# Kernel optimization log

Measured on AMD Instinct MI355X. Metric: run time of the kernel, lower is better.

The kernel has to match this reference:

```python
import jax, jax.numpy as jnp
import numpy as np
from jax import lax

B, N, D = 4, 2048, 1024
MAX_SEQ = 2048
GROUPS = 4  # math.gcd(1024, 4)
LN_EPS = 1e-5


def setup_inputs() -> dict:
    key = jax.random.key(0)
    ks = jax.random.split(key, 12)
    s = 0.02
    return {
        "x": jax.random.normal(ks[0], (B, N, D), jnp.float32),
        "Wq": jax.random.normal(ks[1], (D, D), jnp.float32) * s,
        "Wk": jax.random.normal(ks[2], (D, D), jnp.float32) * s,
        "Wv": jax.random.normal(ks[3], (D, D), jnp.float32) * s,
        "rel_bias": jax.random.normal(ks[4], (1, MAX_SEQ, MAX_SEQ), jnp.float32) * s,
        "conv_w": jax.random.normal(ks[5], (D, D // GROUPS, 3), jnp.float32) * s,
        "conv_b": jnp.zeros((D,), jnp.float32),
        "resg_w": jax.random.normal(ks[6], (D, D), jnp.float32) * s,
        "resg_b": jnp.zeros((D,), jnp.float32),
        "ln_g": jnp.ones((D,), jnp.float32),
        "ln_b": jnp.zeros((D,), jnp.float32),
        "fc1_w": jax.random.normal(ks[7], (D // 2, D), jnp.float32) * s,
        "fc1_b": jnp.zeros((D // 2,), jnp.float32),
        "fc2_w": jax.random.normal(ks[8], (1, D // 2), jnp.float32) * s,
        "fc2_b": jnp.zeros((1,), jnp.float32),
    }


def _forward(x, Wq, Wk, Wv, rel_bias, conv_w, conv_b, resg_w, resg_b,
             ln_g, ln_b, fc1_w, fc1_b, fc2_w, fc2_b):
    b, n, d = x.shape
    scale = 1.0 / jnp.sqrt(jnp.asarray(d, x.dtype))
    q = x @ Wq.T  # [b,n,dk]
    k = x @ Wk.T
    v = x @ Wv.T  # [b,n,dv]
    att = jnp.einsum("bqd,bkd->bqk", q, k) * scale + rel_bias[:, :n, :n]
    causal = jnp.tril(jnp.ones((n, n), bool))
    att = jnp.where(causal, att, jnp.asarray(-jnp.inf, att.dtype))
    att = jax.nn.softmax(att, axis=-1)  # dropout is identity at eval
    att_out = jnp.einsum("bqk,bkd->bqd", att, v)
    # grouped temporal conv over sequence dim: v [b,n,dv] -> NCH [b,dv,n]
    conv = lax.conv_general_dilated(
        v.transpose(0, 2, 1), conv_w, window_strides=(1,), padding=[(1, 1)],
        dimension_numbers=("NCH", "OIH", "NCH"), feature_group_count=GROUPS)
    conv = conv + conv_b[None, :, None]
    out = att_out + conv.transpose(0, 2, 1)
    res = jax.nn.sigmoid(out @ resg_w.T + resg_b)
    out = x + res * out
    mu = out.mean(-1, keepdims=True)
    var = out.var(-1, keepdims=True)
    out = (out - mu) * lax.rsqrt(var + LN_EPS) * ln_g + ln_b
    h = jax.nn.gelu(out @ fc1_w.T + fc1_b, approximate=False)
    return jax.nn.sigmoid(h @ fc2_w.T + fc2_b)


def reference(x, Wq, Wk, Wv, rel_bias, conv_w, conv_b, resg_w, resg_b,
              ln_g, ln_b, fc1_w, fc1_b, fc2_w, fc2_b):
    return _forward(x, Wq, Wk, Wv, rel_bias, conv_w, conv_b, resg_w, resg_b,
                    ln_g, ln_b, fc1_w, fc1_b, fc2_w, fc2_b)
```

## Files before the change

### kernel.cpp

```cpp
#include <hip/hip_runtime.h>
#include <math.h>

#define NSEQ 2048
#define DDIM 1024
#define BSZ  4
#define BM 128
#define BN 128
#define BK 64

typedef short bf16x8 __attribute__((ext_vector_type(8)));
typedef float f32x4 __attribute__((ext_vector_type(4)));
typedef unsigned int u32;
typedef unsigned short u16;

__device__ __forceinline__ u16 f2bf(float f) {
  union { float f; u32 u; } x; x.f = f;
  u32 r = x.u + 0x7FFFu + ((x.u >> 16) & 1u);
  return (u16)(r >> 16);
}
__device__ __forceinline__ float bf2f(u16 h) {
  union { u32 u; float f; } x; x.u = ((u32)h) << 16; return x.f;
}
__device__ __forceinline__ float sigmoidf_(float x) {
  return 1.0f / (1.0f + expf(-x));
}

__device__ __forceinline__ void async_copy16(const u16* g, u16* l) {
  __builtin_amdgcn_global_load_lds(
      (const __attribute__((address_space(1))) u32*)g,
      (__attribute__((address_space(3))) u32*)l, 16, 0, 0);
}

__device__ __forceinline__ void stage_tile(const u16* __restrict__ gsrc, size_t ld,
                                           int k0, u16* lds, int tid) {
  const int wave = tid >> 6, lane = tid & 63;
  const int rr = lane >> 3;
  const int q  = (lane & 7) ^ rr;
#pragma unroll
  for (int j = 0; j < 4; ++j) {
    const int c = j * 4 + wave;
    async_copy16(gsrc + (size_t)(c * 8 + rr) * ld + k0 + q * 8, lds + c * 512);
  }
}

__device__ __forceinline__ void mfma_step(const u16* Al, const u16* Bl,
                                          int wr, int wc, int l16, int quad,
                                          f32x4 acc[4][4]) {
  const int r7 = l16 & 7;
#pragma unroll
  for (int ks = 0; ks < 2; ++ks) {
    const int s = ((ks * 4 + quad) ^ r7) << 3;
    bf16x8 a[4], b[4];
#pragma unroll
    for (int i = 0; i < 4; ++i) {
      a[i] = *(const bf16x8*)(Al + (wr * 64 + i * 16 + l16) * BK + s);
      b[i] = *(const bf16x8*)(Bl + (wc * 64 + i * 16 + l16) * BK + s);
    }
#pragma unroll
    for (int i = 0; i < 4; ++i)
#pragma unroll
      for (int j = 0; j < 4; ++j)
        acc[i][j] = __builtin_amdgcn_mfma_f32_16x16x32_bf16(a[i], b[j], acc[i][j], 0, 0, 0);
  }
}

__device__ __forceinline__ void zero_acc(f32x4 acc[4][4]) {
#pragma unroll
  for (int i = 0; i < 4; ++i)
#pragma unroll
    for (int j = 0; j < 4; ++j) {
      f32x4 z = {0.f, 0.f, 0.f, 0.f};
      acc[i][j] = z;
    }
}

__device__ __forceinline__ void gemm_loop(const u16* A, size_t lda,
                                          const u16* Bt, size_t ldb, int K,
                                          u16* Al, u16* Bl, int tid,
                                          int wr, int wc, int l16, int quad,
                                          f32x4 acc[4][4]) {
  for (int k0 = 0; k0 < K; k0 += BK) {
    __syncthreads();
    stage_tile(A, lda, k0, Al, tid);
    stage_tile(Bt, ldb, k0, Bl, tid);
    __syncthreads();
    mfma_step(Al, Bl, wr, wc, l16, quad, acc);
  }
}

#define ATT_PB 2228224

__global__ __launch_bounds__(256) void k_prep(
    const float* __restrict__ x,  const float* __restrict__ Wq,
    const float* __restrict__ Wk, const float* __restrict__ Wv,
    const float* __restrict__ rw, const float* __restrict__ f1w,
    const float* __restrict__ cw,
    u16* __restrict__ xb,  u16* __restrict__ Wqb, u16* __restrict__ Wkb,
    u16* __restrict__ Wvb, u16* __restrict__ rwb, u16* __restrict__ f1wb,
    u16* __restrict__ cwp, u16* __restrict__ vpad, float* __restrict__ outz)
{
  const int blk = blockIdx.x, tid = threadIdx.x;
  const float* s; u16* d; int base;
  if (blk < 8192)       { s = x;   d = xb;   base = blk; }
  else if (blk < 9216)  { s = Wq;  d = Wqb;  base = blk - 8192; }
  else if (blk < 10240) { s = Wk;  d = Wkb;  base = blk - 9216; }
  else if (blk < 11264) { s = Wv;  d = Wvb;  base = blk - 10240; }
  else if (blk < 12288) { s = rw;  d = rwb;  base = blk - 11264; }
  else if (blk < 12800) { s = f1w; d = f1wb; base = blk - 12288; }
  else if (blk < 13824) {
    const int o = blk - 12800, i = tid;
#pragma unroll
    for (int tap = 0; tap < 3; ++tap)
      cwp[(size_t)o * 768 + tap * 256 + i] = f2bf(cw[(size_t)o * 768 + i * 3 + tap]);
    return;
  } else if (blk < 13832) {
    const int e = blk - 13824, bb = e >> 1, which = e & 1;
    u16* row = vpad + (size_t)bb * 2050 * 1024 + (which ? (size_t)2049 * 1024 : 0);
    ushort4 z = {0, 0, 0, 0};
    ((ushort4*)row)[tid] = z;
    return;
  } else {
    const int e = blk - 13832;
    float4 z = {0.f, 0.f, 0.f, 0.f};
    ((float4*)outz)[e * 256 + tid] = z;
    return;
  }
  const int i = base * 256 + tid;
  const float4 v = ((const float4*)s)[i];
  ushort4 o;
  o.x = f2bf(v.x); o.y = f2bf(v.y); o.z = f2bf(v.z); o.w = f2bf(v.w);
  ((ushort4*)d)[i] = o;
}

__global__ __launch_bounds__(256) void k_qkv(
    const u16* __restrict__ xb, const u16* __restrict__ Wqb,
    const u16* __restrict__ Wkb, const u16* __restrict__ Wvb,
    u16* __restrict__ qb, u16* __restrict__ kb, u16* __restrict__ vpad)
{
  __shared__ u16 Al[BM * BK], Bl[BN * BK];
  const int tid = threadIdx.x, z = blockIdx.z;
  const u16* W = (z == 0) ? Wqb : ((z == 1) ? Wkb : Wvb);
  const int row0 = blockIdx.x * BM, col0 = blockIdx.y * BN;
  const int lane = tid & 63, wave = tid >> 6;
  const int quad = lane >> 4, l16 = lane & 15, wr = wave >> 1, wc = wave & 1;
  f32x4 acc[4][4];
  zero_acc(acc);
  gemm_loop(xb + (size_t)row0 * DDIM, DDIM, W + (size_t)col0 * DDIM, DDIM, DDIM,
            Al, Bl, tid, wr, wc, l16, quad, acc);
#pragma unroll
  for (int mi = 0; mi < 4; ++mi)
#pragma unroll
    for (int r = 0; r < 4; ++r) {
      const int grow = row0 + wr * 64 + mi * 16 + quad * 4 + r;
#pragma unroll
      for (int ni = 0; ni < 4; ++ni) {
        const int gcol = col0 + wc * 64 + ni * 16 + l16;
        const u16 hv = f2bf(acc[mi][ni][r]);
        if (z == 2) {
          const int b = grow >> 11, t = grow & 2047;
          vpad[(size_t)b * 2050 * 1024 + 1024 + (size_t)t * 1024 + gcol] = hv;
        } else {
          (z == 0 ? qb : kb)[(size_t)grow * DDIM + gcol] = hv;
        }
      }
    }
}

__global__ __launch_bounds__(256) void k_vt(const u16* __restrict__ vpad,
                                            u16* __restrict__ vT)
{
  __shared__ u16 tile[64][72];
  const int t0 = blockIdx.x * 64, d0 = blockIdx.y * 64, b = blockIdx.z;
  const int tid = threadIdx.x;
  const u16* vb = vpad + (size_t)b * 2050 * 1024 + 1024;
#pragma unroll
  for (int p = 0; p < 4; ++p) {
    const int r = p * 16 + (tid >> 4), c = (tid & 15) << 2;
    const ushort4 v4 = *(const ushort4*)(vb + (size_t)(t0 + r) * 1024 + d0 + c);
    tile[r][c] = v4.x; tile[r][c + 1] = v4.y; tile[r][c + 2] = v4.z; tile[r][c + 3] = v4.w;
  }
  __syncthreads();
  u16* ob = vT + (size_t)b * DDIM * NSEQ;
#pragma unroll
  for (int p = 0; p < 4; ++p) {
    const int d = p * 16 + (tid >> 4), t = (tid & 15) << 2;
    ushort4 o;
    o.x = tile[t][d]; o.y = tile[t + 1][d]; o.z = tile[t + 2][d]; o.w = tile[t + 3][d];
    *(ushort4*)(ob + (size_t)(d0 + d) * NSEQ + t0 + t) = o;
  }
}

__global__ __launch_bounds__(256) void k_conv(
    const u16* __restrict__ vpad, const u16* __restrict__ cwp,
    const float* __restrict__ cb, u16* __restrict__ convb)
{
  __shared__ u16 Al[BM * BK], Bl[BN * BK];
  const int tid = threadIdx.x;
  const int row0 = blockIdx.x * BM;
  const int col0 = blockIdx.y * BN;
  const int g = col0 >> 8;
  const int b = row0 >> 11, t0 = row0 & 2047;
  const u16* vb = vpad + (size_t)b * 2050 * 1024 + 1024;
  const u16* Bbase = cwp + (size_t)col0 * 768;
  const int lane = tid & 63, wave = tid >> 6;
  const int quad = lane >> 4, l16 = lane & 15, wr = wave >> 1, wc = wave & 1;
  const int rr = lane >> 3;
  const int q  = (lane & 7) ^ rr;
  const int gch = g << 8;
  f32x4 acc[4][4];
  zero_acc(acc);
  for (int k0 = 0; k0 < 768; k0 += BK) {
    __syncthreads();
    const int tap = k0 >> 8;
    const int i0 = k0 & 255;
#pragma unroll
    for (int j = 0; j < 4; ++j) {
      const int c = j * 4 + wave;
      const int r = c * 8 + rr;
      async_copy16(vb + (size_t)(t0 + r - 1 + tap) * 1024 + gch + i0 + q * 8,
                   Al + c * 512);
    }
    stage_tile(Bbase, 768, k0, Bl, tid);
    __syncthreads();
    mfma_step(Al, Bl, wr, wc, l16, quad, acc);
  }
#pragma unroll
  for (int mi = 0; mi < 4; ++mi)
#pragma unroll
    for (int r = 0; r < 4; ++r) {
      const int grow = row0 + wr * 64 + mi * 16 + quad * 4 + r;
#pragma unroll
      for (int ni = 0; ni < 4; ++ni) {
        const int gcol = col0 + wc * 64 + ni * 16 + l16;
        convb[(size_t)grow * DDIM + gcol] = f2bf(cb[gcol] + acc[mi][ni][r]);
      }
    }
}

__global__ __launch_bounds__(256) void k_scores(
    const u16* __restrict__ qb, const u16* __restrict__ kb,
    const float* __restrict__ rb, float* __restrict__ attp)
{
  __shared__ u16 Al[BM * BK], Bl[BN * BK];
  const int b = blockIdx.x, t = blockIdx.y, tid = threadIdx.x;
  int it = 0;
  while ((it + 1) * (it + 2) / 2 <= t) ++it;
  const int jt = t - it * (it + 1) / 2;
  const int row0 = it * BM, col0 = jt * BN;
  const int lane = tid & 63, wave = tid >> 6;
  const int quad = lane >> 4, l16 = lane & 15, wr = wave >> 1, wc = wave & 1;
  f32x4 acc[4][4];
  zero_acc(acc);
  gemm_loop(qb + ((size_t)b * NSEQ + row0) * DDIM, DDIM,
            kb + ((size_t)b * NSEQ + col0) * DDIM, DDIM, DDIM,
            Al, Bl, tid, wr, wc, l16, quad, acc);
  float* abase = attp + (size_t)b * ATT_PB + (size_t)(it * (it + 1) / 2) * 16384;
  const int ldp = (it + 1) * 128;
#pragma unroll
  for (int mi = 0; mi < 4; ++mi)
#pragma unroll
    for (int r = 0; r < 4; ++r) {
      const int ri = wr * 64 + mi * 16 + quad * 4 + r;
      const int gi = row0 + ri;
#pragma unroll
      for (int ni = 0; ni < 4; ++ni) {
        const int j = col0 + wc * 64 + ni * 16 + l16;
        abase[(size_t)ri * ldp + j] =
            acc[mi][ni][r] * 0.03125f + rb[(size_t)gi * NSEQ + j];
      }
    }
}

__global__ __launch_bounds__(256) void k_softmax(const float* __restrict__ attp,
                                                 u16* __restrict__ pp)
{
  const int i = blockIdx.x, b = blockIdx.y;
  const int it = i >> 7;
  const int wlen = (it + 1) << 7;
  const size_t rbase = (size_t)b * ATT_PB +
                       (size_t)(it * (it + 1) / 2) * 16384 + (size_t)(i & 127) * wlen;
  const float* row = attp + rbase;
  u16* orow = pp + rbase;
  const int valid = i + 1;
  const int tid = threadIdx.x;
  const int lane = tid & 63, wid = tid >> 6;

  float v[8];
  float m = -1e30f;
#pragma unroll
  for (int t = 0; t < 8; ++t) {
    const int idx = tid + (t << 8);
    v[t] = (idx < valid) ? row[idx] : -1e30f;
    m = fmaxf(m, v[t]);
  }
#pragma unroll
  for (int off = 32; off; off >>= 1) m = fmaxf(m, __shfl_xor(m, off));
  __shared__ float red[4];
  if (lane == 0) red[wid] = m;
  __syncthreads();
  m = fmaxf(fmaxf(red[0], red[1]), fmaxf(red[2], red[3]));
  __syncthreads();

  float s = 0.f;
#pragma unroll
  for (int t = 0; t < 8; ++t) {
    const int idx = tid + (t << 8);
    float e = (idx < valid) ? expf(v[t] - m) : 0.f;
    v[t] = e;
    s += e;
  }
#pragma unroll
  for (int off = 32; off; off >>= 1) s += __shfl_xor(s, off);
  if (lane == 0) red[wid] = s;
  __syncthreads();
  s = red[0] + red[1] + red[2] + red[3];
  const float inv = 1.0f / s;
#pragma unroll
  for (int t = 0; t < 8; ++t) {
    const int idx = tid + (t << 8);
    if (idx < wlen) orow[idx] = f2bf(v[t] * inv);
  }
}

__global__ __launch_bounds__(256) void k_pv(
    const u16* __restrict__ pp, const u16* __restrict__ vT,
    const u16* __restrict__ convb, u16* __restrict__ buf1b)
{
  __shared__ u16 Al[BM * BK], Bl[BN * BK];
  const int it = 15 - blockIdx.x, nt = blockIdx.y, b = blockIdx.z;
  const int tid = threadIdx.x;
  const int row0 = it * BM, col0 = nt * BN;
  const int K = (it + 1) * BM;
  const int lane = tid & 63, wave = tid >> 6;
  const int quad = lane >> 4, l16 = lane & 15, wr = wave >> 1, wc = wave & 1;
  f32x4 acc[4][4];
  zero_acc(acc);
  gemm_loop(pp + (size_t)b * ATT_PB + (size_t)(it * (it + 1) / 2) * 16384, K,
            vT + ((size_t)b * DDIM + col0) * NSEQ, NSEQ, K,
            Al, Bl, tid, wr, wc, l16, quad, acc);
  const size_t obase = (size_t)b * NSEQ * DDIM;
#pragma unroll
  for (int mi = 0; mi < 4; ++mi)
#pragma unroll
    for (int r = 0; r < 4; ++r) {
      const int grow = row0 + wr * 64 + mi * 16 + quad * 4 + r;
#pragma unroll
      for (int ni = 0; ni < 4; ++ni) {
        const int gcol = col0 + wc * 64 + ni * 16 + l16;
        const size_t idx = obase + (size_t)grow * DDIM + gcol;
        buf1b[idx] = f2bf(acc[mi][ni][r] + bf2f(convb[idx]));
      }
    }
}

__global__ __launch_bounds__(256) void k_resgate(
    const u16* __restrict__ buf1b, const u16* __restrict__ rwb,
    const float* __restrict__ rbias, const u16* __restrict__ xb,
    u16* __restrict__ buf2)
{
  __shared__ u16 Al[BM * BK], Bl[BN * BK];
  const int tid = threadIdx.x;
  const int row0 = blockIdx.x * BM, col0 = blockIdx.y * BN;
  const int lane = tid & 63, wave = tid >> 6;
  const int quad = lane >> 4, l16 = lane & 15, wr = wave >> 1, wc = wave & 1;
  f32x4 acc[4][4];
  zero_acc(acc);
  gemm_loop(buf1b + (size_t)row0 * DDIM, DDIM, rwb + (size_t)col0 * DDIM, DDIM,
            DDIM, Al, Bl, tid, wr, wc, l16, quad, acc);
#pragma unroll
  for (int mi = 0; mi < 4; ++mi)
#pragma unroll
    for (int r = 0; r < 4; ++r) {
      const int grow = row0 + wr * 64 + mi * 16 + quad * 4 + r;
#pragma unroll
      for (int ni = 0; ni < 4; ++ni) {
        const int gcol = col0 + wc * 64 + ni * 16 + l16;
        const size_t idx = (size_t)grow * DDIM + gcol;
        const float gate = sigmoidf_(acc[mi][ni][r] + rbias[gcol]);
        buf2[idx] = f2bf(bf2f(xb[idx]) + gate * bf2f(buf1b[idx]));
      }
    }
}

__global__ __launch_bounds__(256) void k_ln(
    const u16* __restrict__ buf, const float* __restrict__ gw,
    const float* __restrict__ gb, u16* __restrict__ outb)
{
  const int row = blockIdx.x;
  const u16* p = buf + (size_t)row * DDIM;
  const int tid = threadIdx.x;
  const int lane = tid & 63, wid = tid >> 6;
  const int c = tid << 2;
  const ushort4 raw = *(const ushort4*)(p + c);
  float4 val;
  val.x = bf2f(raw.x); val.y = bf2f(raw.y); val.z = bf2f(raw.z); val.w = bf2f(raw.w);
  float s = val.x + val.y + val.z + val.w;
  float s2 = val.x * val.x + val.y * val.y + val.z * val.z + val.w * val.w;
#pragma unroll
  for (int off = 32; off; off >>= 1) {
    s += __shfl_xor(s, off);
    s2 += __shfl_xor(s2, off);
  }
  __shared__ float r1[4], r2[4];
  if (lane == 0) { r1[wid] = s; r2[wid] = s2; }
  __syncthreads();
  s = r1[0] + r1[1] + r1[2] + r1[3];
  s2 = r2[0] + r2[1] + r2[2] + r2[3];
  const float mean = s * (1.0f / DDIM);
  const float var = s2 * (1.0f / DDIM) - mean * mean;
  const float rstd = rsqrtf(var + 1e-5f);
  const float4 g4 = *(const float4*)(gw + c);
  const float4 b4 = *(const float4*)(gb + c);
  ushort4 o;
  o.x = f2bf((val.x - mean) * rstd * g4.x + b4.x);
  o.y = f2bf((val.y - mean) * rstd * g4.y + b4.y);
  o.z = f2bf((val.z - mean) * rstd * g4.z + b4.z);
  o.w = f2bf((val.w - mean) * rstd * g4.w + b4.w);
  *(ushort4*)(outb + (size_t)row * DDIM + c) = o;
}

__global__ __launch_bounds__(256) void k_fc1(
    const u16* __restrict__ A, const u16* __restrict__ W,
    const float* __restrict__ bias, const float* __restrict__ w2,
    float* __restrict__ outacc)
{
  __shared__ u16 Al[BM * BK], Bl[BN * BK];
  const int tid = threadIdx.x;
  const int row0 = blockIdx.x * BM, col0 = blockIdx.y * BN;
  const int lane = tid & 63, wave = tid >> 6;
  const int quad = lane >> 4, l16 = lane & 15, wr = wave >> 1, wc = wave & 1;
  f32x4 acc[4][4];
  zero_acc(acc);
  gemm_loop(A + (size_t)row0 * DDIM, DDIM, W + (size_t)col0 * DDIM, DDIM, DDIM,
            Al, Bl, tid, wr, wc, l16, quad, acc);
  float w4[4], b4[4];
#pragma unroll
  for (int ni = 0; ni < 4; ++ni) {
    const int gcol = col0 + wc * 64 + ni * 16 + l16;
    w4[ni] = w2[gcol];
    b4[ni] = bias[gcol];
  }
#pragma unroll
  for (int mi = 0; mi < 4; ++mi)
#pragma unroll
    for (int r = 0; r < 4; ++r) {
      const int grow = row0 + wr * 64 + mi * 16 + quad * 4 + r;
      float part = 0.f;
#pragma unroll
      for (int ni = 0; ni < 4; ++ni) {
        const float t = acc[mi][ni][r] + b4[ni];
        const float g = 0.5f * t * (1.0f + erff(t * 0.70710678118654752f));
        part = fmaf(g, w4[ni], part);
      }
#pragma unroll
      for (int off = 1; off < 16; off <<= 1) part += __shfl_xor(part, off, 16);
      if (l16 == 0) atomicAdd(outacc + grow, part);
    }
}

__global__ __launch_bounds__(256) void k_fin(float* __restrict__ out,
                                             const float* __restrict__ b2)
{
  const int i = blockIdx.x * 256 + threadIdx.x;
  out[i] = sigmoidf_(out[i] + b2[0]);
}

extern "C" void kernel_launch(void* const* d_in, const int* in_sizes, int n_in,
                              void* d_out, int out_size, void* d_ws, size_t ws_size,
                              hipStream_t stream) {
  const float* x    = (const float*)d_in[0];
  const float* Wq   = (const float*)d_in[1];
  const float* Wk   = (const float*)d_in[2];
  const float* Wv   = (const float*)d_in[3];
  const float* rb   = (const float*)d_in[4];
  const float* cw   = (const float*)d_in[5];
  const float* cb   = (const float*)d_in[6];
  const float* rw   = (const float*)d_in[7];
  const float* rbias= (const float*)d_in[8];
  const float* lng  = (const float*)d_in[9];
  const float* lnb  = (const float*)d_in[10];
  const float* f1w  = (const float*)d_in[11];
  const float* f1b  = (const float*)d_in[12];
  const float* f2w  = (const float*)d_in[13];
  const float* f2b  = (const float*)d_in[14];
  float* out = (float*)d_out;
  char* w8 = (char*)d_ws;

  u16* xb    = (u16*)(w8 + 0);
  u16* Wqb   = (u16*)(w8 + 16777216);
  u16* Wkb   = (u16*)(w8 + 18874368);
  u16* Wvb   = (u16*)(w8 + 20971520);
  u16* rwb   = (u16*)(w8 + 23068672);
  u16* f1wb  = (u16*)(w8 + 25165824);
  u16* cwp   = (u16*)(w8 + 26214400);
  u16* qb    = (u16*)(w8 + 27787264);
  u16* kb    = (u16*)(w8 + 44564480);
  u16* vpad  = (u16*)(w8 + 61341696);
  u16* vT    = (u16*)(w8 + 78135296);
  float* attp= (float*)(w8 + 94912512);
  u16* convb = (u16*)(w8 + 130564096);
  u16* pp    = (u16*)(w8 + 27787264);
  u16* buf1b = (u16*)(w8 + 45613056);
  u16* buf2  = (u16*)(w8 + 94912512);
  u16* ln16  = (u16*)(w8 + 78135296);

  k_prep   <<<dim3(13840),     256, 0, stream>>>(x, Wq, Wk, Wv, rw, f1w, cw,
                                                 xb, Wqb, Wkb, Wvb, rwb, f1wb,
                                                 cwp, vpad, out);
  k_qkv    <<<dim3(64, 8, 3),  256, 0, stream>>>(xb, Wqb, Wkb, Wvb, qb, kb, vpad);
  k_vt     <<<dim3(32, 16, 4), 256, 0, stream>>>(vpad, vT);
  k_conv   <<<dim3(64, 8),     256, 0, stream>>>(vpad, cwp, cb, convb);
  k_scores <<<dim3(4, 136),    256, 0, stream>>>(qb, kb, rb, attp);
  k_softmax<<<dim3(NSEQ, BSZ), 256, 0, stream>>>(attp, pp);
  k_pv     <<<dim3(16, 8, 4),  256, 0, stream>>>(pp, vT, convb, buf1b);
  k_resgate<<<dim3(64, 8),     256, 0, stream>>>(buf1b, rwb, rbias, xb, buf2);
  k_ln     <<<dim3(BSZ * NSEQ),256, 0, stream>>>(buf2, lng, lnb, ln16);
  k_fc1    <<<dim3(64, 4),     256, 0, stream>>>(ln16, f1wb, f1b, f2w, out);
  k_fin    <<<dim3(32),        256, 0, stream>>>(out, f2b);
}
```

Measured before the change: 384.2 us.

## Fold LayerNorm into resgate stats and fc1 epilogue; store scores in fp16

The standalone LayerNorm kernel is removed. Row sum and sum-of-squares are accumulated with atomics in the resgate epilogue. The LN gain is folded into fc1 weights, with per-column sums of W·g and W·b precomputed, so fc1 applies mean and rstd algebraically in its epilogue on the raw residual output. Attention scores are written as fp16 instead of fp32, halving the score buffer traffic between the scores and softmax kernels. The costs are extra atomics, precision risk from computing variance as E[x²]-μ² and from fp16 scores, and an extra pass to zero the stats buffers.

New measurement: 383.1 us. About the same (-0.3%).

```diff
diff --git a/kernel.cpp b/kernel.cpp
--- a/kernel.cpp
+++ b/kernel.cpp
@@ -20,6 +20,12 @@
 }
 __device__ __forceinline__ float bf2f(u16 h) {
   union { u32 u; float f; } x; x.u = ((u32)h) << 16; return x.f;
+}
+__device__ __forceinline__ u16 f2h(float f) {
+  union { _Float16 h; u16 u; } x; x.h = (_Float16)f; return x.u;
+}
+__device__ __forceinline__ float h2f(u16 u) {
+  union { _Float16 h; u16 u; } x; x.u = u; return (float)x.h;
 }
 __device__ __forceinline__ float sigmoidf_(float x) {
   return 1.0f / (1.0f + expf(-x));
@@ -94,39 +100,69 @@
     const float* __restrict__ x,  const float* __restrict__ Wq,
     const float* __restrict__ Wk, const float* __restrict__ Wv,
     const float* __restrict__ rw, const float* __restrict__ f1w,
-    const float* __restrict__ cw,
+    const float* __restrict__ cw, const float* __restrict__ lng,
+    const float* __restrict__ lnb, const float* __restrict__ f1b,
     u16* __restrict__ xb,  u16* __restrict__ Wqb, u16* __restrict__ Wkb,
     u16* __restrict__ Wvb, u16* __restrict__ rwb, u16* __restrict__ f1wb,
-    u16* __restrict__ cwp, u16* __restrict__ vpad, float* __restrict__ outz)
+    u16* __restrict__ cwp, u16* __restrict__ vpad, float* __restrict__ outz,
+    float* __restrict__ lsum, float* __restrict__ s1, float* __restrict__ tb1)
 {
   const int blk = blockIdx.x, tid = threadIdx.x;
-  const float* s; u16* d; int base;
+  if (blk >= 12800) {
+    if (blk < 13824) {
+      const int o = blk - 12800, i = tid;
+#pragma unroll
+      for (int tap = 0; tap < 3; ++tap)
+        cwp[(size_t)o * 768 + tap * 256 + i] = f2bf(cw[(size_t)o * 768 + i * 3 + tap]);
+    } else if (blk < 13832) {
+      const int e = blk - 13824, bb = e >> 1, which = e & 1;
+      u16* row = vpad + (size_t)bb * 2050 * 1024 + (which ? (size_t)2049 * 1024 : 0);
+      ushort4 z = {0, 0, 0, 0};
+      ((ushort4*)row)[tid] = z;
+    } else if (blk < 13840) {
+      const int e = blk - 13832;
+      float4 z = {0.f, 0.f, 0.f, 0.f};
+      ((float4*)outz)[e * 256 + tid] = z;
+    } else if (blk < 13856) {
+      const int e = blk - 13840;
+      float4 z = {0.f, 0.f, 0.f, 0.f};
+      ((float4*)lsum)[e * 256 + tid] = z;
+    } else {
+      const int c = blk - 13856;
+      const float4 w = ((const float4*)f1w)[c * 256 + tid];
+      const float4 g = ((const float4*)lng)[tid];
+      const float4 bb = ((const float4*)lnb)[tid];
+      float s = w.x * g.x + w.y * g.y + w.z * g.z + w.w * g.w;
+      float t = w.x * bb.x + w.y * bb.y + w.z * bb.z + w.w * bb.w;
+      const int lane = tid & 63, wid = tid >> 6;
+#pragma unroll
+      for (int off = 32; off; off >>= 1) {
+        s += __shfl_xor(s, off);
+        t += __shfl_xor(t, off);
+      }
+      __shared__ float r1[4], r2[4];
+      if (lane == 0) { r1[wid] = s; r2[wid] = t; }
+      __syncthreads();
+      if (tid == 0) {
+        s1[c]  = r1[0] + r1[1] + r1[2] + r1[3];
+        tb1[c] = r2[0] + r2[1] + r2[2] + r2[3] + f1b[c];
+      }
+    }
+    return;
+  }
+  const float* s; u16* d; int base; bool scale_g = false;
   if (blk < 8192)       { s = x;   d = xb;   base = blk; }
   else if (blk < 9216)  { s = Wq;  d = Wqb;  base = blk - 8192; }
   else if (blk < 10240) { s = Wk;  d = Wkb;  base = blk - 9216; }
   else if (blk < 11264) { s = Wv;  d = Wvb;  base = blk - 10240; }
   else if (blk < 12288) { s = rw;  d = rwb;  base = blk - 11264; }
-  else if (blk < 12800) { s = f1w; d = f1wb; base = blk - 12288; }
-  else if (blk < 13824) {
-    const int o = blk - 12800, i = tid;
-#pragma unroll
-    for (int tap = 0; tap < 3; ++tap)
-      cwp[(size_t)o * 768 + tap * 256 + i] = f2bf(cw[(size_t)o * 768 + i * 3 + tap]);
-    return;
-  } else if (blk < 13832) {
-    const int e = blk - 13824, bb = e >> 1, which = e & 1;
-    u16* row = vpad + (size_t)bb * 2050 * 1024 + (which ? (size_t)2049 * 1024 : 0);
-    ushort4 z = {0, 0, 0, 0};
-    ((ushort4*)row)[tid] = z;
-    return;
-  } else {
-    const int e = blk - 13832;
-    float4 z = {0.f, 0.f, 0.f, 0.f};
-    ((float4*)outz)[e * 256 + tid] = z;
-    return;
-  }
+  else                  { s = f1w; d = f1wb; base = blk - 12288; scale_g = true; }
   const int i = base * 256 + tid;
-  const float4 v = ((const float4*)s)[i];
+  float4 v = ((const float4*)s)[i];
+  if (scale_g) {
+    const float4 g = ((const float4*)lng)[i & 255];
+    v.x *= g.x; v.y *= g.y; v.z *= g.z; v.w *= g.w;
+  }
   ushort4 o;
   o.x = f2bf(v.x); o.y = f2bf(v.y); o.z = f2bf(v.z); o.w = f2bf(v.w);
   ((ushort4*)d)[i] = o;
@@ -239,7 +275,7 @@
 
 __global__ __launch_bounds__(256) void k_scores(
     const u16* __restrict__ qb, const u16* __restrict__ kb,
-    const float* __restrict__ rb, float* __restrict__ attp)
+    const float* __restrict__ rb, u16* __restrict__ attp)
 {
   __shared__ u16 Al[BM * BK], Bl[BN * BK];
   const int b = blockIdx.x, t = blockIdx.y, tid = threadIdx.x;
@@ -254,7 +290,7 @@
   gemm_loop(qb + ((size_t)b * NSEQ + row0) * DDIM, DDIM,
             kb + ((size_t)b * NSEQ + col0) * DDIM, DDIM, DDIM,
             Al, Bl, tid, wr, wc, l16, quad, acc);
-  float* abase = attp + (size_t)b * ATT_PB + (size_t)(it * (it + 1) / 2) * 16384;
+  u16* abase = attp + (size_t)b * ATT_PB + (size_t)(it * (it + 1) / 2) * 16384;
   const int ldp = (it + 1) * 128;
 #pragma unroll
   for (int mi = 0; mi < 4; ++mi)
@@ -266,12 +302,12 @@
       for (int ni = 0; ni < 4; ++ni) {
         const int j = col0 + wc * 64 + ni * 16 + l16;
         abase[(size_t)ri * ldp + j] =
-            acc[mi][ni][r] * 0.03125f + rb[(size_t)gi * NSEQ + j];
-      }
-    }
-}
-
-__global__ __launch_bounds__(256) void k_softmax(const float* __restrict__ attp,
+            f2h(acc[mi][ni][r] * 0.03125f + rb[(size_t)gi * NSEQ + j]);
+      }
+    }
+}
+
+__global__ __launch_bounds__(256) void k_softmax(const u16* __restrict__ attp,
                                                  u16* __restrict__ pp)
 {
   const int i = blockIdx.x, b = blockIdx.y;
@@ -279,7 +315,7 @@
   const int wlen = (it + 1) << 7;
   const size_t rbase = (size_t)b * ATT_PB +
                        (size_t)(it * (it + 1) / 2) * 16384 + (size_t)(i & 127) * wlen;
-  const float* row = attp + rbase;
+  const u16* row = attp + rbase;
   u16* orow = pp + rbase;
   const int valid = i + 1;
   const int tid = threadIdx.x;
@@ -290,7 +326,7 @@
 #pragma unroll
   for (int t = 0; t < 8; ++t) {
     const int idx = tid + (t << 8);
-    v[t] = (idx < valid) ? row[idx] : -1e30f;
+    v[t] = (idx < valid) ? h2f(row[idx]) : -1e30f;
     m = fmaxf(m, v[t]);
   }
 #pragma unroll
@@ -356,7 +392,7 @@
 __global__ __launch_bounds__(256) void k_resgate(
     const u16* __restrict__ buf1b, const u16* __restrict__ rwb,
     const float* __restrict__ rbias, const u16* __restrict__ xb,
-    u16* __restrict__ buf2)
+    u16* __restrict__ buf2, float* __restrict__ lsum, float* __restrict__ lsum2)
 {
   __shared__ u16 Al[BM * BK], Bl[BN * BK];
   const int tid = threadIdx.x;
@@ -372,57 +408,35 @@
 #pragma unroll
     for (int r = 0; r < 4; ++r) {
       const int grow = row0 + wr * 64 + mi * 16 + quad * 4 + r;
+      float rs = 0.f, rs2 = 0.f;
 #pragma unroll
       for (int ni = 0; ni < 4; ++ni) {
         const int gcol = col0 + wc * 64 + ni * 16 + l16;
         const size_t idx = (size_t)grow * DDIM + gcol;
         const float gate = sigmoidf_(acc[mi][ni][r] + rbias[gcol]);
-        buf2[idx] = f2bf(bf2f(xb[idx]) + gate * bf2f(buf1b[idx]));
-      }
-    }
-}
-
-__global__ __launch_bounds__(256) void k_ln(
-    const u16* __restrict__ buf, const float* __restrict__ gw,
-    const float* __restrict__ gb, u16* __restrict__ outb)
-{
-  const int row = blockIdx.x;
-  const u16* p = buf + (size_t)row * DDIM;
-  const int tid = threadIdx.x;
-  const int lane = tid & 63, wid = tid >> 6;
-  const int c = tid << 2;
-  const ushort4 raw = *(const ushort4*)(p + c);
-  float4 val;
-  val.x = bf2f(raw.x); val.y = bf2f(raw.y); val.z = bf2f(raw.z); val.w = bf2f(raw.w);
-  float s = val.x + val.y + val.z + val.w;
-  float s2 = val.x * val.x + val.y * val.y + val.z * val.z + val.w * val.w;
-#pragma unroll
-  for (int off = 32; off; off >>= 1) {
-    s += __shfl_xor(s, off);
-    s2 += __shfl_xor(s2, off);
-  }
-  __shared__ float r1[4], r2[4];
-  if (lane == 0) { r1[wid] = s; r2[wid] = s2; }
-  __syncthreads();
-  s = r1[0] + r1[1] + r1[2] + r1[3];
-  s2 = r2[0] + r2[1] + r2[2] + r2[3];
-  const float mean = s * (1.0f / DDIM);
-  const float var = s2 * (1.0f / DDIM) - mean * mean;
-  const float rstd = rsqrtf(var + 1e-5f);
-  const float4 g4 = *(const float4*)(gw + c);
-  const float4 b4 = *(const float4*)(gb + c);
-  ushort4 o;
-  o.x = f2bf((val.x - mean) * rstd * g4.x + b4.x);
-  o.y = f2bf((val.y - mean) * rstd * g4.y + b4.y);
-  o.z = f2bf((val.z - mean) * rstd * g4.z + b4.z);
-  o.w = f2bf((val.w - mean) * rstd * g4.w + b4.w);
-  *(ushort4*)(outb + (size_t)row * DDIM + c) = o;
+        const u16 vb = f2bf(bf2f(xb[idx]) + gate * bf2f(buf1b[idx]));
+        buf2[idx] = vb;
+        const float vr = bf2f(vb);
+        rs += vr;
+        rs2 += vr * vr;
+      }
+#pragma unroll
+      for (int off = 1; off < 16; off <<= 1) {
+        rs  += __shfl_xor(rs, off, 16);
+        rs2 += __shfl_xor(rs2, off, 16);
+      }
+      if (l16 == 0) {
+        atomicAdd(lsum + grow, rs);
+        atomicAdd(lsum2 + grow, rs2);
+      }
+    }
 }
 
 __global__ __launch_bounds__(256) void k_fc1(
     const u16* __restrict__ A, const u16* __restrict__ W,
-    const float* __restrict__ bias, const float* __restrict__ w2,
-    float* __restrict__ outacc)
+    const float* __restrict__ s1, const float* __restrict__ tb1,
+    const float* __restrict__ w2, const float* __restrict__ lsum,
+    const float* __restrict__ lsum2, float* __restrict__ outacc)
 {
   __shared__ u16 Al[BM * BK], Bl[BN * BK];
   const int tid = threadIdx.x;
@@ -433,23 +447,28 @@
   zero_acc(acc);
   gemm_loop(A + (size_t)row0 * DDIM, DDIM, W + (size_t)col0 * DDIM, DDIM, DDIM,
             Al, Bl, tid, wr, wc, l16, quad, acc);
-  float w4[4], b4[4];
+  float w4[4], s14[4], tb14[4];
 #pragma unroll
   for (int ni = 0; ni < 4; ++ni) {
     const int gcol = col0 + wc * 64 + ni * 16 + l16;
     w4[ni] = w2[gcol];
-    b4[ni] = bias[gcol];
+    s14[ni] = s1[gcol];
+    tb14[ni] = tb1[gcol];
   }
 #pragma unroll
   for (int mi = 0; mi < 4; ++mi)
 #pragma unroll
     for (int r = 0; r < 4; ++r) {
       const int grow = row0 + wr * 64 + mi * 16 + quad * 4 + r;
+      const float mu = lsum[grow] * (1.0f / DDIM);
+      const float var = lsum2[grow] * (1.0f / DDIM) - mu * mu;
+      const float rstd = rsqrtf(var + 1e-5f);
+      const float nms = -rstd * mu;
       float part = 0.f;
 #pragma unroll
       for (int ni = 0; ni < 4; ++ni) {
-        const float t = acc[mi][ni][r] + b4[ni];
-        const float g = 0.5f * t * (1.0f + erff(t * 0.70710678118654752f));
+        const float pre = fmaf(rstd, acc[mi][ni][r], fmaf(nms, s14[ni], tb14[ni]));
+        const float g = 0.5f * pre * (1.0f + erff(pre * 0.70710678118654752f));
         part = fmaf(g, w4[ni], part);
       }
 #pragma unroll
@@ -497,24 +516,29 @@
   u16* kb    = (u16*)(w8 + 44564480);
   u16* vpad  = (u16*)(w8 + 61341696);
   u16* vT    = (u16*)(w8 + 78135296);
-  float* attp= (float*)(w8 + 94912512);
+  u16* attp  = (u16*)(w8 + 94912512);
   u16* convb = (u16*)(w8 + 130564096);
+  float* s1  = (float*)(w8 + 147341312);
+  float* tb1 = (float*)(w8 + 147343360);
+  float* lsum  = (float*)(w8 + 147345408);
+  float* lsum2 = (float*)(w8 + 147378176);
   u16* pp    = (u16*)(w8 + 27787264);
   u16* buf1b = (u16*)(w8 + 45613056);
-  u16* buf2  = (u16*)(w8 + 94912512);
-  u16* ln16  = (u16*)(w8 + 78135296);
-
-  k_prep   <<<dim3(13840),     256, 0, stream>>>(x, Wq, Wk, Wv, rw, f1w, cw,
+  u16* buf2  = (u16*)(w8 + 112746496);
+
+  k_prep   <<<dim3(14368),     256, 0, stream>>>(x, Wq, Wk, Wv, rw, f1w, cw,
+                                                 lng, lnb, f1b,
                                                  xb, Wqb, Wkb, Wvb, rwb, f1wb,
-                                                 cwp, vpad, out);
+                                                 cwp, vpad, out, lsum, s1, tb1);
   k_qkv    <<<dim3(64, 8, 3),  256, 0, stream>>>(xb, Wqb, Wkb, Wvb, qb, kb, vpad);
   k_vt     <<<dim3(32, 16, 4), 256, 0, stream>>>(vpad, vT);
   k_conv   <<<dim3(64, 8),     256, 0, stream>>>(vpad, cwp, cb, convb);
   k_scores <<<dim3(4, 136),    256, 0, stream>>>(qb, kb, rb, attp);
   k_softmax<<<dim3(NSEQ, BSZ), 256, 0, stream>>>(attp, pp);
   k_pv     <<<dim3(16, 8, 4),  256, 0, stream>>>(pp, vT, convb, buf1b);
-  k_resgate<<<dim3(64, 8),     256, 0, stream>>>(buf1b, rwb, rbias, xb, buf2);
-  k_ln     <<<dim3(BSZ * NSEQ),256, 0, stream>>>(buf2, lng, lnb, ln16);
-  k_fc1    <<<dim3(64, 4),     256, 0, stream>>>(ln16, f1wb, f1b, f2w, out);
+  k_resgate<<<dim3(64, 8),     256, 0, stream>>>(buf1b, rwb, rbias, xb, buf2,
+                                                 lsum, lsum2);
+  k_fc1    <<<dim3(64, 4),     256, 0, stream>>>(buf2, f1wb, s1, tb1, f2w,
+                                                 lsum, lsum2, out);
   k_fin    <<<dim3(32),        256, 0, stream>>>(out, f2b);
 }
```
